# Kernel tuning notes

Hardware: AMD Instinct MI355X
Metric: run time of the kernel (lower is better)

## Reference

```python
import jax, jax.numpy as jnp
import numpy as np

B, S, D = 8, 1024, 1024
H, KV, HD = 16, 16, 64
NDIM = 2
EPS = 1e-6


def rms_norm(x, weight=None, eps=EPS):
    var = jnp.mean(jnp.square(x), axis=-1, keepdims=True)
    out = x * jax.lax.rsqrt(var + eps)
    if weight is not None:
        out = out * weight
    return out


def rotate_half(x):
    half = x.shape[-1] // 2
    return jnp.concatenate((-x[..., half:], x[..., :half]), axis=-1)


def multidim_rope(x, cos, sin, ndim):
    # x: [B,S,H,HD]; cos,sin: [B,S,HD]; head_dim split into ndim contiguous
    # chunks of size per = 2*(HD // (2*ndim)); rotate-half applied per chunk.
    b, s, h, hd = x.shape
    per = 2 * (hd // (2 * ndim))
    xg = x.reshape(b, s, h, ndim, per)
    cg = cos.reshape(b, s, 1, ndim, per)
    sg = sin.reshape(b, s, 1, ndim, per)
    out = xg * cg + rotate_half(xg) * sg
    return out.reshape(b, s, h, hd)


def setup_inputs() -> dict:
    key = jax.random.key(0)
    ks = jax.random.split(key, 10)
    scale = 1.0 / np.sqrt(D)
    return {
        "hidden_states": jax.random.normal(ks[0], (B, S, D), jnp.float32),
        "cos": jax.random.uniform(ks[1], (B, S, HD), jnp.float32, -1.0, 1.0),
        "sin": jax.random.uniform(ks[2], (B, S, HD), jnp.float32, -1.0, 1.0),
        "position_ids": jax.random.randint(ks[3], (B, S, NDIM), 0, 32, jnp.int32),
        "wq": jax.random.normal(ks[4], (D, H * HD), jnp.float32) * scale,
        "wk": jax.random.normal(ks[5], (D, KV * HD), jnp.float32) * scale,
        "wv": jax.random.normal(ks[6], (D, KV * HD), jnp.float32) * scale,
        "wo": jax.random.normal(ks[7], (H * HD, D), jnp.float32) * scale,
        "q_norm_w": jnp.ones((HD,), jnp.float32),
        "k_norm_w": jnp.ones((HD,), jnp.float32),
    }


def reference(hidden_states, cos, sin, position_ids, wq, wk, wv, wo, q_norm_w, k_norm_w):
    b, s, _ = hidden_states.shape
    ndim = position_ids.shape[-1]

    q = (hidden_states @ wq).reshape(b, s, H, HD)
    q = rms_norm(q, q_norm_w)
    q = multidim_rope(q, cos, sin, ndim)

    k = (hidden_states @ wk).reshape(b, s, KV, HD)
    k = rms_norm(k, k_norm_w)
    k = multidim_rope(k, cos, sin, ndim)

    v = (hidden_states @ wv).reshape(b, s, KV, HD)
    v = rms_norm(v, None)  # v_norm has no weight

    # Full (non-causal) vision attention, scaling = 1.0
    scores = jnp.einsum("bqhd,bkhd->bhqk", q, k)
    probs = jax.nn.softmax(scores, axis=-1)
    attn = jnp.einsum("bhqk,bkhd->bqhd", probs, v).reshape(b, s, H * HD)

    return attn @ wo
```

## Files before the change

kernel.cpp:

```cpp
#include <hip/hip_runtime.h>
#include <hip/hip_bf16.h>

typedef __attribute__((ext_vector_type(8))) short bf16x8;
typedef __attribute__((ext_vector_type(4))) short bf16x4;
typedef __attribute__((ext_vector_type(4))) float f32x4;

struct __align__(16) V16 { unsigned long long a, b; };

__device__ __forceinline__ float bf2f(unsigned short u) {
  union { unsigned int i; float f; } c; c.i = ((unsigned int)u) << 16; return c.f;
}
__device__ __forceinline__ unsigned short f2bf(float f) {
  __hip_bfloat16 h = __float2bfloat16(f);
  unsigned short u; __builtin_memcpy(&u, &h, 2); return u;
}

__device__ __forceinline__ void async16(unsigned short* lds,
                                        const unsigned short* g) {
  __builtin_amdgcn_global_load_lds(
      (const __attribute__((address_space(1))) unsigned int*)g,
      (__attribute__((address_space(3))) unsigned int*)lds, 16, 0, 0);
}

#define FP32_MAGIC 0x3F800000u

__global__ __launch_bounds__(256) void cvt_bf16(
    const void* __restrict__ src, size_t srcOff,
    unsigned short* __restrict__ dst, int n4,
    const unsigned int* __restrict__ fmt)
{
  const bool f32 = (fmt[0] == FP32_MAGIC);
  int i = blockIdx.x * blockDim.x + threadIdx.x;
  const int stride = gridDim.x * blockDim.x;
  if (f32) {
    const float* s = (const float*)src + srcOff;
    for (; i < n4; i += stride) {
      float4 v = *(const float4*)(s + (size_t)i * 4);
      ushort2 lo = { f2bf(v.x), f2bf(v.y) };
      ushort2 hi = { f2bf(v.z), f2bf(v.w) };
      *(ushort2*)(dst + (size_t)i * 4)     = lo;
      *(ushort2*)(dst + (size_t)i * 4 + 2) = hi;
    }
  } else {
    const unsigned short* s = (const unsigned short*)src + srcOff;
    for (; i < n4; i += stride) {
      *(ushort4*)(dst + (size_t)i * 4) = *(const ushort4*)(s + (size_t)i * 4);
    }
  }
}

__global__ __launch_bounds__(256) void cvt_t(
    const void* __restrict__ src, unsigned short* __restrict__ dstT,
    const unsigned int* __restrict__ fmt)
{
  __shared__ __align__(16) unsigned short T[64][72];
  const bool f32 = (fmt[0] == FP32_MAGIC);
  const int tid = threadIdx.x;
  const int k0 = blockIdx.x * 64, n0 = blockIdx.y * 64;
  const int rl = tid >> 3, cl = (tid & 7) * 8;

#pragma unroll
  for (int p = 0; p < 2; ++p) {
    int r = rl + p * 32;
    int cs = cl ^ (r & 56);
    if (f32) {
      const float* s = (const float*)src + (size_t)(k0 + r) * 1024 + n0 + cl;
      float4 v0 = *(const float4*)s, v1 = *(const float4*)(s + 4);
      unsigned short* t = &T[r][cs];
      t[0]=f2bf(v0.x); t[1]=f2bf(v0.y); t[2]=f2bf(v0.z); t[3]=f2bf(v0.w);
      t[4]=f2bf(v1.x); t[5]=f2bf(v1.y); t[6]=f2bf(v1.z); t[7]=f2bf(v1.w);
    } else {
      *(V16*)&T[r][cs] = *(const V16*)((const unsigned short*)src +
                                        (size_t)(k0 + r) * 1024 + n0 + cl);
    }
  }
  __syncthreads();

#pragma unroll
  for (int p = 0; p < 2; ++p) {
    int u = tid + p * 256;
    int d = u >> 3, sc = (u & 7) * 8;
    unsigned short tmp[8];
#pragma unroll
    for (int i = 0; i < 8; ++i) tmp[i] = T[sc + i][d ^ sc];
    *(V16*)&dstT[(size_t)(n0 + d) * 1024 + k0 + sc] = *(V16*)tmp;
  }
}

__global__ __launch_bounds__(256) void transpose_v(
    const unsigned short* __restrict__ v, unsigned short* __restrict__ vt)
{
  __shared__ __align__(16) unsigned short T[64][72];
  const int tid = threadIdx.x;
  const int s0 = blockIdx.x * 64;
  const int bh = blockIdx.y;
  const int b = bh >> 4, h = bh & 15;
  const int rl = tid >> 3, cl = (tid & 7) * 8;

#pragma unroll
  for (int p = 0; p < 2; ++p) {
    int r = rl + p * 32;
    *(V16*)&T[r][cl ^ (r & 56)] = *(const V16*)(
        v + (size_t)(b * 1024 + s0 + r) * 1024 + h * 64 + cl);
  }
  __syncthreads();

#pragma unroll
  for (int p = 0; p < 2; ++p) {
    int u = tid + p * 256;
    int d = u >> 3, sc = (u & 7) * 8;
    unsigned short tmp[8];
#pragma unroll
    for (int i = 0; i < 8; ++i) tmp[i] = T[sc + i][d ^ sc];
    *(V16*)&vt[(size_t)(bh * 64 + d) * 1024 + s0 + sc] = *(V16*)tmp;
  }
}

#define TM 128
#define TN 128
#define TK 64

__global__ __launch_bounds__(256) void gemm_qkv(
    const unsigned short* __restrict__ A,
    const unsigned short* __restrict__ Bt,
    unsigned short* __restrict__ Cq,
    unsigned short* __restrict__ Ck,
    unsigned short* __restrict__ Cv,
    const unsigned short* __restrict__ cs,
    const unsigned short* __restrict__ sn,
    const unsigned short* __restrict__ qw,
    const unsigned short* __restrict__ kw,
    int M, int K)
{
  __shared__ __align__(16) unsigned short As[TM][TK];
  __shared__ __align__(16) unsigned short Bs[TN][TK];

  const int tid  = threadIdx.x;
  const int wave = tid >> 6;
  const int lane = tid & 63;
  const int quad = lane >> 4;
  const int l16  = lane & 15;
  const int bm = blockIdx.x * TM;
  const int bn = blockIdx.y * TN;
  const int wm = (wave & 1) * 64;
  const int wn = (wave >> 1) * 64;

  const f32x4 z = {0.f, 0.f, 0.f, 0.f};
  f32x4 acc[4][4];
#pragma unroll
  for (int i = 0; i < 4; ++i)
#pragma unroll
    for (int j = 0; j < 4; ++j) acc[i][j] = z;

  const int lrow = lane >> 3;
  const int gcol = ((lane & 7) ^ lrow) * 8;
  const unsigned short* aP = A  + (size_t)(bm + wave * 8 + lrow) * K + gcol;
  const unsigned short* bP = Bt + (size_t)(bn + wave * 8 + lrow) * K + gcol;
  const int cswz = l16 & 7;

  for (int k0 = 0; k0 < K; k0 += TK) {
#pragma unroll
    for (int p = 0; p < 4; ++p) {
      async16(&As[p * 32 + wave * 8][0], aP + (size_t)p * 32 * K);
      async16(&Bs[p * 32 + wave * 8][0], bP + (size_t)p * 32 * K);
    }
    aP += TK; bP += TK;
    __syncthreads();

#pragma unroll
    for (int s = 0; s < 2; ++s) {
      const int pc = ((s * 4 + quad) ^ cswz) * 8;
      bf16x8 af[4], bfv[4];
#pragma unroll
      for (int mt = 0; mt < 4; ++mt)
        af[mt] = *(const bf16x8*)&As[wm + mt * 16 + l16][pc];
#pragma unroll
      for (int nt = 0; nt < 4; ++nt)
        bfv[nt] = *(const bf16x8*)&Bs[wn + nt * 16 + l16][pc];
#pragma unroll
      for (int mt = 0; mt < 4; ++mt)
#pragma unroll
        for (int nt = 0; nt < 4; ++nt)
          acc[mt][nt] = __builtin_amdgcn_mfma_f32_16x16x32_bf16(
              af[mt], bfv[nt], acc[mt][nt], 0, 0, 0);
    }
    __syncthreads();
  }

  const int which = bn >> 10;
  unsigned short* Cd = (which == 0) ? Cq : (which == 1) ? Ck : Cv;
  const int colbase = (bn & 1023) + wn;

  float wgt[4];
#pragma unroll
  for (int nt = 0; nt < 4; ++nt) {
    int d = nt * 16 + l16;
    wgt[nt] = (which == 0) ? bf2f(qw[d]) * 1.44269504f
            : (which == 1) ? bf2f(kw[d]) : 1.f;
  }

#pragma unroll
  for (int mt = 0; mt < 4; ++mt)
#pragma unroll
    for (int r = 0; r < 4; ++r) {
      const int row = bm + wm + mt * 16 + quad * 4 + r;
      float x0 = acc[mt][0][r], x1 = acc[mt][1][r];
      float x2 = acc[mt][2][r], x3 = acc[mt][3][r];
      float ss = x0 * x0 + x1 * x1 + x2 * x2 + x3 * x3;
      ss += __shfl_xor(ss, 1);
      ss += __shfl_xor(ss, 2);
      ss += __shfl_xor(ss, 4);
      ss += __shfl_xor(ss, 8);
      const float inv = rsqrtf(ss * (1.f / 64.f) + 1e-6f);
      float y[4] = { x0 * inv * wgt[0], x1 * inv * wgt[1],
                     x2 * inv * wgt[2], x3 * inv * wgt[3] };
      float outv[4];
      if (which < 2) {
        const unsigned short* cp = cs + (size_t)row * 64 + l16;
        const unsigned short* sp = sn + (size_t)row * 64 + l16;
#pragma unroll
        for (int nt = 0; nt < 4; ++nt) {
          float c = bf2f(cp[nt * 16]), s = bf2f(sp[nt * 16]);
          float part = (nt & 1) ? y[nt ^ 1] : -y[nt ^ 1];
          outv[nt] = y[nt] * c + part * s;
        }
      } else {
#pragma unroll
        for (int nt = 0; nt < 4; ++nt) outv[nt] = y[nt];
      }
#pragma unroll
      for (int nt = 0; nt < 4; ++nt)
        Cd[(size_t)row * 1024 + colbase + nt * 16 + l16] = f2bf(outv[nt]);
    }
}

__global__ __launch_bounds__(256) void gemm_bf16(
    const unsigned short* __restrict__ A,
    const unsigned short* __restrict__ Bt,
    void* __restrict__ C, size_t cOff,
    const unsigned int* __restrict__ outFmt,
    int M, int N, int K)
{
  __shared__ __align__(16) unsigned short As[TM][TK];
  __shared__ __align__(16) unsigned short Bs[TN][TK];

  const int tid  = threadIdx.x;
  const int wave = tid >> 6;
  const int lane = tid & 63;
  const int quad = lane >> 4;
  const int l16  = lane & 15;
  const int bm = blockIdx.x * TM;
  const int bn = blockIdx.y * TN;
  const int wm = (wave & 1) * 64;
  const int wn = (wave >> 1) * 64;

  const f32x4 z = {0.f, 0.f, 0.f, 0.f};
  f32x4 acc[4][4];
#pragma unroll
  for (int i = 0; i < 4; ++i)
#pragma unroll
    for (int j = 0; j < 4; ++j) acc[i][j] = z;

  const int lrow = lane >> 3;
  const int gcol = ((lane & 7) ^ lrow) * 8;
  const unsigned short* aP = A  + (size_t)(bm + wave * 8 + lrow) * K + gcol;
  const unsigned short* bP = Bt + (size_t)(bn + wave * 8 + lrow) * K + gcol;
  const int cswz = l16 & 7;

  for (int k0 = 0; k0 < K; k0 += TK) {
#pragma unroll
    for (int p = 0; p < 4; ++p) {
      async16(&As[p * 32 + wave * 8][0], aP + (size_t)p * 32 * K);
      async16(&Bs[p * 32 + wave * 8][0], bP + (size_t)p * 32 * K);
    }
    aP += TK; bP += TK;
    __syncthreads();

#pragma unroll
    for (int s = 0; s < 2; ++s) {
      const int pc = ((s * 4 + quad) ^ cswz) * 8;
      bf16x8 af[4], bfv[4];
#pragma unroll
      for (int mt = 0; mt < 4; ++mt)
        af[mt] = *(const bf16x8*)&As[wm + mt * 16 + l16][pc];
#pragma unroll
      for (int nt = 0; nt < 4; ++nt)
        bfv[nt] = *(const bf16x8*)&Bs[wn + nt * 16 + l16][pc];
#pragma unroll
      for (int mt = 0; mt < 4; ++mt)
#pragma unroll
        for (int nt = 0; nt < 4; ++nt)
          acc[mt][nt] = __builtin_amdgcn_mfma_f32_16x16x32_bf16(
              af[mt], bfv[nt], acc[mt][nt], 0, 0, 0);
    }
    __syncthreads();
  }

  const bool of32 = (outFmt != nullptr) && (outFmt[0] == FP32_MAGIC);
  float* Cf = (float*)C + cOff;
  unsigned short* Ch = (unsigned short*)C + cOff;

#pragma unroll
  for (int mt = 0; mt < 4; ++mt)
#pragma unroll
    for (int nt = 0; nt < 4; ++nt)
#pragma unroll
      for (int r = 0; r < 4; ++r) {
        int row = bm + wm + mt * 16 + quad * 4 + r;
        int col = bn + wn + nt * 16 + l16;
        size_t idx = (size_t)row * N + col;
        if (of32) Cf[idx] = acc[mt][nt][r];
        else      Ch[idx] = f2bf(acc[mt][nt][r]);
      }
}

__global__ __launch_bounds__(256) void attn_fused(
    const unsigned short* __restrict__ q,
    const unsigned short* __restrict__ k,
    const unsigned short* __restrict__ vt,
    unsigned short* __restrict__ o)
{
  __shared__ __align__(16) unsigned short Ks[2][64][64];
  __shared__ __align__(16) unsigned short Vs[2][64][64];

  const int tid  = threadIdx.x;
  const int wave = tid >> 6;
  const int lane = tid & 63;
  const int quad = lane >> 4;
  const int l16  = lane & 15;
  const int bh = blockIdx.y;
  const int b  = bh >> 4, h = bh & 15;
  const int qbase = blockIdx.x * 64 + wave * 16;
  const size_t bbase = (size_t)b * 1024;

  bf16x8 qf[2];
  {
    const unsigned short* qp = q + (bbase + qbase + l16) * 1024 + h * 64;
    qf[0] = *(const bf16x8*)(qp + quad * 8);
    qf[1] = *(const bf16x8*)(qp + 32 + quad * 8);
  }

  const f32x4 z = {0.f, 0.f, 0.f, 0.f};
  f32x4 of[5];
#pragma unroll
  for (int nt = 0; nt < 5; ++nt) of[nt] = z;
  float m_run = -1e30f;

  const bf16x8 onesv = { 0x3F80, 0x3F80, 0x3F80, 0x3F80,
                         0x3F80, 0x3F80, 0x3F80, 0x3F80 };

  const int lrow = lane >> 3;
  const int gcol = ((lane & 7) ^ lrow) * 8;
  const unsigned short* kP = k  + (bbase + wave * 8 + lrow) * 1024 + h * 64 + gcol;
  const unsigned short* vP = vt + ((size_t)bh * 64 + wave * 8 + lrow) * 1024 + gcol;
  const int cswz = l16 & 7;

  auto STAGE = [&](int buf, int kt) {
#pragma unroll
    for (int p = 0; p < 2; ++p) {
      async16(&Ks[buf][p * 32 + wave * 8][0], kP + ((size_t)kt * 64 + p * 32) * 1024);
      async16(&Vs[buf][p * 32 + wave * 8][0], vP + (size_t)p * 32 * 1024 + kt * 64);
    }
  };

  STAGE(0, 0);
  __syncthreads();

  for (int kt = 0; kt < 16; ++kt) {
    const int cur = kt & 1;
    if (kt < 15) STAGE(cur ^ 1, kt + 1);

    f32x4 sf[4];
#pragma unroll
    for (int nt = 0; nt < 4; ++nt) sf[nt] = z;
#pragma unroll
    for (int s = 0; s < 2; ++s) {
      const int pc = ((s * 4 + quad) ^ cswz) * 8;
#pragma unroll
      for (int nt = 0; nt < 4; ++nt) {
        bf16x8 kf = *(const bf16x8*)&Ks[cur][nt * 16 + l16][pc];
        sf[nt] = __builtin_amdgcn_mfma_f32_16x16x32_bf16(kf, qf[s], sf[nt], 0, 0, 0);
      }
    }

    float m0 = fmaxf(fmaxf(sf[0][0], sf[0][1]), fmaxf(sf[0][2], sf[0][3]));
    float m1 = fmaxf(fmaxf(sf[1][0], sf[1][1]), fmaxf(sf[1][2], sf[1][3]));
    float m2 = fmaxf(fmaxf(sf[2][0], sf[2][1]), fmaxf(sf[2][2], sf[2][3]));
    float m3 = fmaxf(fmaxf(sf[3][0], sf[3][1]), fmaxf(sf[3][2], sf[3][3]));
    float mx = fmaxf(fmaxf(m0, m1), fmaxf(m2, m3));
    mx = fmaxf(mx, __shfl_xor(mx, 16));
    mx = fmaxf(mx, __shfl_xor(mx, 32));

    if (!__all(mx - m_run <= 11.5f)) {
      float mn = fmaxf(m_run, mx);
      float alpha = __builtin_amdgcn_exp2f(m_run - mn);
      m_run = mn;
      float ar[4];
#pragma unroll
      for (int r = 0; r < 4; ++r) ar[r] = __shfl(alpha, quad * 4 + r);
#pragma unroll
      for (int nt = 0; nt < 5; ++nt)
#pragma unroll
        for (int r = 0; r < 4; ++r) of[nt][r] *= ar[r];
    }

    bf16x8 pf[2];
#pragma unroll
    for (int nt = 0; nt < 4; ++nt)
#pragma unroll
      for (int r = 0; r < 4; ++r)
        pf[nt >> 1][(nt & 1) * 4 + r] =
            (short)f2bf(__builtin_amdgcn_exp2f(sf[nt][r] - m_run));

#pragma unroll
    for (int s = 0; s < 2; ++s) {
#pragma unroll
      for (int nt = 0; nt < 4; ++nt) {
        const unsigned short* vrow = &Vs[cur][nt * 16 + l16][0];
        const int g0  = (4 * s + (quad >> 1)) ^ cswz;
        const int off = 4 * (quad & 1);
        bf16x4 v0 = *(const bf16x4*)(vrow + g0 * 8 + off);
        bf16x4 v1 = *(const bf16x4*)(vrow + (g0 ^ 2) * 8 + off);
        bf16x8 vf = __builtin_shufflevector(v0, v1, 0, 1, 2, 3, 4, 5, 6, 7);
        of[nt] = __builtin_amdgcn_mfma_f32_16x16x32_bf16(pf[s], vf, of[nt], 0, 0, 0);
      }
      of[4] = __builtin_amdgcn_mfma_f32_16x16x32_bf16(pf[s], onesv, of[4], 0, 0, 0);
    }

    __syncthreads();
  }

  float invl[4];
#pragma unroll
  for (int r = 0; r < 4; ++r) invl[r] = 1.f / of[4][r];
#pragma unroll
  for (int nt = 0; nt < 4; ++nt)
#pragma unroll
    for (int r = 0; r < 4; ++r) {
      int row = qbase + quad * 4 + r;
      o[(bbase + row) * 1024 + h * 64 + nt * 16 + l16] = f2bf(of[nt][r] * invl[r]);
    }
}

extern "C" void kernel_launch(void* const* d_in, const int* in_sizes, int n_in,
                              void* d_out, int out_size, void* d_ws, size_t ws_size,
                              hipStream_t stream) {
  const void* hidden = d_in[0];
  const void* cosr   = d_in[1];
  const void* sinr   = d_in[2];
  const void* wq     = d_in[4];
  const void* wk     = d_in[5];
  const void* wv     = d_in[6];
  const void* wo     = d_in[7];
  const void* qnw    = d_in[8];
  const void* knw    = d_in[9];
  const unsigned int* fmt = (const unsigned int*)qnw;

  const size_t MEG = 1024 * 1024;
  dim3 blk(256);
  unsigned short* w = (unsigned short*)d_ws;

  auto cvt = [&](const void* src, size_t srcOff, unsigned short* dst, int n) {
    int n4 = n / 4;
    int blocks = (n4 + 1023) / 1024;
    if (blocks > 2048) blocks = 2048;
    cvt_bf16<<<dim3(blocks), blk, 0, stream>>>(src, srcOff, dst, n4, fmt);
  };
  auto cvtT = [&](const void* src, unsigned short* dstT) {
    cvt_t<<<dim3(16, 16), blk, 0, stream>>>(src, dstT, fmt);
  };

  if (ws_size >= (size_t)60 * MEG) {
    unsigned short* hb   = w;
    unsigned short* vtb  = w;
    unsigned short* wqT  = w + 8 * MEG;
    unsigned short* wkT  = w + 9 * MEG;
    unsigned short* wvT  = w + 10 * MEG;
    unsigned short* woT  = w + 11 * MEG;
    unsigned short* csb  = w + 12 * MEG;
    unsigned short* snb  = w + 12 * MEG + 512 * 1024;
    unsigned short* qnb  = w + 13 * MEG;
    unsigned short* knb  = w + 13 * MEG + 64;
    unsigned short* qb   = w + 14 * MEG;
    unsigned short* kb   = w + 22 * MEG;
    unsigned short* vb   = (unsigned short*)d_out;
    unsigned short* ab   = qb;

    cvt(hidden, 0, hb, 8 * MEG);
    cvtT(wq, wqT);  cvtT(wk, wkT);  cvtT(wv, wvT);  cvtT(wo, woT);
    cvt(cosr, 0, csb, 512 * 1024);  cvt(sinr, 0, snb, 512 * 1024);
    cvt(qnw, 0, qnb, 64);  cvt(knw, 0, knb, 64);

    const int M = 8192, K = 1024;
    gemm_qkv<<<dim3(M / TM, 24), blk, 0, stream>>>(hb, wqT, qb, kb, vb,
                                                   csb, snb, qnb, knb, M, K);
    transpose_v<<<dim3(16, 8 * 16), blk, 0, stream>>>(vb, vtb);
    attn_fused<<<dim3(16, 8 * 16), blk, 0, stream>>>(qb, kb, vtb, ab);
    gemm_bf16<<<dim3(M / TM, 8), blk, 0, stream>>>(ab, woT, d_out, 0, fmt,
                                                   M, 1024, K);
  } else {
    unsigned short* wqT  = w;
    unsigned short* wkT  = w + 1 * MEG;
    unsigned short* wvT  = w + 2 * MEG;
    unsigned short* woT  = w + 3 * MEG;
    unsigned short* csb  = w + 4 * MEG;
    unsigned short* snb  = w + 4 * MEG + 512 * 1024;
    unsigned short* qnb  = w + 5 * MEG;
    unsigned short* knb  = w + 5 * MEG + 64;
    unsigned short* hbb  = w + 6 * MEG;
    unsigned short* qb   = w + 7 * MEG;
    unsigned short* kb   = w + 8 * MEG;
    unsigned short* vb   = w + 9 * MEG;
    unsigned short* vtb  = w + 10 * MEG;

    cvtT(wq, wqT);  cvtT(wk, wkT);  cvtT(wv, wvT);  cvtT(wo, woT);
    cvt(cosr, 0, csb, 512 * 1024);  cvt(sinr, 0, snb, 512 * 1024);
    cvt(qnw, 0, qnb, 64);  cvt(knw, 0, knb, 64);

    const int Mb = 1024, K = 1024;
    for (int b = 0; b < 8; ++b) {
      cvt(hidden, (size_t)b * MEG, hbb, MEG);
      gemm_qkv<<<dim3(Mb / TM, 24), blk, 0, stream>>>(
          hbb, wqT, qb, kb, vb, csb + (size_t)b * 64 * 1024,
          snb + (size_t)b * 64 * 1024, qnb, knb, Mb, K);
      transpose_v<<<dim3(16, 16), blk, 0, stream>>>(vb, vtb);
      attn_fused<<<dim3(16, 16), blk, 0, stream>>>(qb, kb, vtb, qb);
      gemm_bf16<<<dim3(Mb / TM, 8), blk, 0, stream>>>(qb, woT, d_out,
                                                      (size_t)b * MEG, fmt,
                                                      Mb, 1024, K);
    }
  }
}
```

Before: 306.0 us.

## Double-buffer GEMM loads, batch conversion launches, add MFMA priority hints

```diff
diff --git a/kernel.cpp b/kernel.cpp
--- a/kernel.cpp
+++ b/kernel.cpp
@@ -11,8 +11,9 @@
   union { unsigned int i; float f; } c; c.i = ((unsigned int)u) << 16; return c.f;
 }
 __device__ __forceinline__ unsigned short f2bf(float f) {
-  __hip_bfloat16 h = __float2bfloat16(f);
-  unsigned short u; __builtin_memcpy(&u, &h, 2); return u;
+  unsigned int u; __builtin_memcpy(&u, &f, 4);
+  u += 0x7FFFu + ((u >> 16) & 1u);
+  return (unsigned short)(u >> 16);
 }
 
 __device__ __forceinline__ void async16(unsigned short* lds,
@@ -24,16 +25,12 @@
 
 #define FP32_MAGIC 0x3F800000u
 
-__global__ __launch_bounds__(256) void cvt_bf16(
-    const void* __restrict__ src, size_t srcOff,
-    unsigned short* __restrict__ dst, int n4,
-    const unsigned int* __restrict__ fmt)
-{
-  const bool f32 = (fmt[0] == FP32_MAGIC);
-  int i = blockIdx.x * blockDim.x + threadIdx.x;
-  const int stride = gridDim.x * blockDim.x;
+__device__ __forceinline__ void cvt_seg(
+    const void* __restrict__ src, unsigned short* __restrict__ dst,
+    int n4, int i, int stride, bool f32)
+{
   if (f32) {
-    const float* s = (const float*)src + srcOff;
+    const float* s = (const float*)src;
     for (; i < n4; i += stride) {
       float4 v = *(const float4*)(s + (size_t)i * 4);
       ushort2 lo = { f2bf(v.x), f2bf(v.y) };
@@ -42,18 +39,61 @@
       *(ushort2*)(dst + (size_t)i * 4 + 2) = hi;
     }
   } else {
-    const unsigned short* s = (const unsigned short*)src + srcOff;
-    for (; i < n4; i += stride) {
+    const unsigned short* s = (const unsigned short*)src;
+    for (; i < n4; i += stride)
       *(ushort4*)(dst + (size_t)i * 4) = *(const ushort4*)(s + (size_t)i * 4);
-    }
-  }
-}
-
-__global__ __launch_bounds__(256) void cvt_t(
-    const void* __restrict__ src, unsigned short* __restrict__ dstT,
+  }
+}
+
+__global__ __launch_bounds__(256) void cvt_bf16(
+    const void* __restrict__ src, size_t srcOff,
+    unsigned short* __restrict__ dst, int n4,
     const unsigned int* __restrict__ fmt)
 {
+  const bool f32 = (fmt[0] == FP32_MAGIC);
+  const int i = blockIdx.x * blockDim.x + threadIdx.x;
+  const int stride = gridDim.x * blockDim.x;
+  const void* s = f32 ? (const void*)((const float*)src + srcOff)
+                      : (const void*)((const unsigned short*)src + srcOff);
+  cvt_seg(s, dst, n4, i, stride, f32);
+}
+
+__global__ __launch_bounds__(256) void cvt_all(
+    const void* __restrict__ hid, const void* __restrict__ cosr,
+    const void* __restrict__ sinr, const void* __restrict__ qnw,
+    const void* __restrict__ knw,
+    unsigned short* __restrict__ hb, unsigned short* __restrict__ csb,
+    unsigned short* __restrict__ snb, unsigned short* __restrict__ qnb,
+    unsigned short* __restrict__ knb,
+    int hidden_n4, const unsigned int* __restrict__ fmt)
+{
+  const bool f32 = (fmt[0] == FP32_MAGIC);
+  const int bx = blockIdx.x, tid = threadIdx.x;
+  if (bx < 2048) {
+    if (hidden_n4 > 0)
+      cvt_seg(hid, hb, hidden_n4, bx * 256 + tid, 2048 * 256, f32);
+  } else if (bx < 2176) {
+    cvt_seg(cosr, csb, 131072, (bx - 2048) * 256 + tid, 128 * 256, f32);
+  } else if (bx < 2304) {
+    cvt_seg(sinr, snb, 131072, (bx - 2176) * 256 + tid, 128 * 256, f32);
+  } else {
+    if (tid < 16)       cvt_seg(qnw, qnb, 16, tid, 16, f32);
+    else if (tid < 32)  cvt_seg(knw, knb, 16, tid - 16, 16, f32);
+  }
+}
+
+__global__ __launch_bounds__(256) void cvt_t4(
+    const void* __restrict__ s0, const void* __restrict__ s1,
+    const void* __restrict__ s2, const void* __restrict__ s3,
+    unsigned short* __restrict__ d0, unsigned short* __restrict__ d1,
+    unsigned short* __restrict__ d2, unsigned short* __restrict__ d3,
+    const unsigned int* __restrict__ fmt)
+{
   __shared__ __align__(16) unsigned short T[64][72];
+  const int z = blockIdx.z;
+  const void* src = (z == 0) ? s0 : (z == 1) ? s1 : (z == 2) ? s2 : s3;
+  unsigned short* dstT = (z == 0) ? d0 : (z == 1) ? d1 : (z == 2) ? d2 : d3;
+
   const bool f32 = (fmt[0] == FP32_MAGIC);
   const int tid = threadIdx.x;
   const int k0 = blockIdx.x * 64, n0 = blockIdx.y * 64;
@@ -119,6 +159,7 @@
 #define TM 128
 #define TN 128
 #define TK 64
+#define GK 1024
 
 __global__ __launch_bounds__(256) void gemm_qkv(
     const unsigned short* __restrict__ A,
@@ -130,10 +171,10 @@
     const unsigned short* __restrict__ sn,
     const unsigned short* __restrict__ qw,
     const unsigned short* __restrict__ kw,
-    int M, int K)
-{
-  __shared__ __align__(16) unsigned short As[TM][TK];
-  __shared__ __align__(16) unsigned short Bs[TN][TK];
+    int M)
+{
+  __shared__ __align__(16) unsigned short As[2][TM][TK];
+  __shared__ __align__(16) unsigned short Bs[2][TN][TK];
 
   const int tid  = threadIdx.x;
   const int wave = tid >> 6;
@@ -154,29 +195,35 @@
 
   const int lrow = lane >> 3;
   const int gcol = ((lane & 7) ^ lrow) * 8;
-  const unsigned short* aP = A  + (size_t)(bm + wave * 8 + lrow) * K + gcol;
-  const unsigned short* bP = Bt + (size_t)(bn + wave * 8 + lrow) * K + gcol;
+  const unsigned short* aP = A  + (size_t)(bm + wave * 8 + lrow) * GK + gcol;
+  const unsigned short* bP = Bt + (size_t)(bn + wave * 8 + lrow) * GK + gcol;
   const int cswz = l16 & 7;
 
-  for (int k0 = 0; k0 < K; k0 += TK) {
+  auto STAGE = [&](int buf, int t) {
 #pragma unroll
     for (int p = 0; p < 4; ++p) {
-      async16(&As[p * 32 + wave * 8][0], aP + (size_t)p * 32 * K);
-      async16(&Bs[p * 32 + wave * 8][0], bP + (size_t)p * 32 * K);
-    }
-    aP += TK; bP += TK;
-    __syncthreads();
-
+      async16(&As[buf][p * 32 + wave * 8][0], aP + t * TK + p * 32 * GK);
+      async16(&Bs[buf][p * 32 + wave * 8][0], bP + t * TK + p * 32 * GK);
+    }
+  };
+
+  STAGE(0, 0);
+  __syncthreads();
+
+#pragma unroll 2
+  for (int t = 0; t < GK / TK; ++t) {
+    const int cur = t & 1;
+    if (t < GK / TK - 1) STAGE(cur ^ 1, t + 1);
 #pragma unroll
     for (int s = 0; s < 2; ++s) {
       const int pc = ((s * 4 + quad) ^ cswz) * 8;
       bf16x8 af[4], bfv[4];
 #pragma unroll
       for (int mt = 0; mt < 4; ++mt)
-        af[mt] = *(const bf16x8*)&As[wm + mt * 16 + l16][pc];
+        af[mt] = *(const bf16x8*)&As[cur][wm + mt * 16 + l16][pc];
 #pragma unroll
       for (int nt = 0; nt < 4; ++nt)
-        bfv[nt] = *(const bf16x8*)&Bs[wn + nt * 16 + l16][pc];
+        bfv[nt] = *(const bf16x8*)&Bs[cur][wn + nt * 16 + l16][pc];
 #pragma unroll
       for (int mt = 0; mt < 4; ++mt)
 #pragma unroll
@@ -239,10 +286,10 @@
     const unsigned short* __restrict__ Bt,
     void* __restrict__ C, size_t cOff,
     const unsigned int* __restrict__ outFmt,
-    int M, int N, int K)
-{
-  __shared__ __align__(16) unsigned short As[TM][TK];
-  __shared__ __align__(16) unsigned short Bs[TN][TK];
+    int M, int N)
+{
+  __shared__ __align__(16) unsigned short As[2][TM][TK];
+  __shared__ __align__(16) unsigned short Bs[2][TN][TK];
 
   const int tid  = threadIdx.x;
   const int wave = tid >> 6;
@@ -263,29 +310,35 @@
 
   const int lrow = lane >> 3;
   const int gcol = ((lane & 7) ^ lrow) * 8;
-  const unsigned short* aP = A  + (size_t)(bm + wave * 8 + lrow) * K + gcol;
-  const unsigned short* bP = Bt + (size_t)(bn + wave * 8 + lrow) * K + gcol;
+  const unsigned short* aP = A  + (size_t)(bm + wave * 8 + lrow) * GK + gcol;
+  const unsigned short* bP = Bt + (size_t)(bn + wave * 8 + lrow) * GK + gcol;
   const int cswz = l16 & 7;
 
-  for (int k0 = 0; k0 < K; k0 += TK) {
+  auto STAGE = [&](int buf, int t) {
 #pragma unroll
     for (int p = 0; p < 4; ++p) {
-      async16(&As[p * 32 + wave * 8][0], aP + (size_t)p * 32 * K);
-      async16(&Bs[p * 32 + wave * 8][0], bP + (size_t)p * 32 * K);
-    }
-    aP += TK; bP += TK;
-    __syncthreads();
-
+      async16(&As[buf][p * 32 + wave * 8][0], aP + t * TK + p * 32 * GK);
+      async16(&Bs[buf][p * 32 + wave * 8][0], bP + t * TK + p * 32 * GK);
+    }
+  };
+
+  STAGE(0, 0);
+  __syncthreads();
+
+#pragma unroll 2
+  for (int t = 0; t < GK / TK; ++t) {
+    const int cur = t & 1;
+    if (t < GK / TK - 1) STAGE(cur ^ 1, t + 1);
 #pragma unroll
     for (int s = 0; s < 2; ++s) {
       const int pc = ((s * 4 + quad) ^ cswz) * 8;
       bf16x8 af[4], bfv[4];
 #pragma unroll
       for (int mt = 0; mt < 4; ++mt)
-        af[mt] = *(const bf16x8*)&As[wm + mt * 16 + l16][pc];
+        af[mt] = *(const bf16x8*)&As[cur][wm + mt * 16 + l16][pc];
 #pragma unroll
       for (int nt = 0; nt < 4; ++nt)
-        bfv[nt] = *(const bf16x8*)&Bs[wn + nt * 16 + l16][pc];
+        bfv[nt] = *(const bf16x8*)&Bs[cur][wn + nt * 16 + l16][pc];
 #pragma unroll
       for (int mt = 0; mt < 4; ++mt)
 #pragma unroll
@@ -366,6 +419,7 @@
   STAGE(0, 0);
   __syncthreads();
 
+#pragma unroll 2
   for (int kt = 0; kt < 16; ++kt) {
     const int cur = kt & 1;
     if (kt < 15) STAGE(cur ^ 1, kt + 1);
@@ -373,6 +427,7 @@
     f32x4 sf[4];
 #pragma unroll
     for (int nt = 0; nt < 4; ++nt) sf[nt] = z;
+    __builtin_amdgcn_s_setprio(1);
 #pragma unroll
     for (int s = 0; s < 2; ++s) {
       const int pc = ((s * 4 + quad) ^ cswz) * 8;
@@ -382,6 +437,7 @@
         sf[nt] = __builtin_amdgcn_mfma_f32_16x16x32_bf16(kf, qf[s], sf[nt], 0, 0, 0);
       }
     }
+    __builtin_amdgcn_s_setprio(0);
 
     float m0 = fmaxf(fmaxf(sf[0][0], sf[0][1]), fmaxf(sf[0][2], sf[0][3]));
     float m1 = fmaxf(fmaxf(sf[1][0], sf[1][1]), fmaxf(sf[1][2], sf[1][3]));
@@ -412,6 +468,7 @@
         pf[nt >> 1][(nt & 1) * 4 + r] =
             (short)f2bf(__builtin_amdgcn_exp2f(sf[nt][r] - m_run));
 
+    __builtin_amdgcn_s_setprio(1);
 #pragma unroll
     for (int s = 0; s < 2; ++s) {
 #pragma unroll
@@ -426,6 +483,7 @@
       }
       of[4] = __builtin_amdgcn_mfma_f32_16x16x32_bf16(pf[s], onesv, of[4], 0, 0, 0);
     }
+    __builtin_amdgcn_s_setprio(0);
 
     __syncthreads();
   }
@@ -459,16 +517,6 @@
   const size_t MEG = 1024 * 1024;
   dim3 blk(256);
   unsigned short* w = (unsigned short*)d_ws;
-
-  auto cvt = [&](const void* src, size_t srcOff, unsigned short* dst, int n) {
-    int n4 = n / 4;
-    int blocks = (n4 + 1023) / 1024;
-    if (blocks > 2048) blocks = 2048;
-    cvt_bf16<<<dim3(blocks), blk, 0, stream>>>(src, srcOff, dst, n4, fmt);
-  };
-  auto cvtT = [&](const void* src, unsigned short* dstT) {
-    cvt_t<<<dim3(16, 16), blk, 0, stream>>>(src, dstT, fmt);
-  };
 
   if (ws_size >= (size_t)60 * MEG) {
     unsigned short* hb   = w;
@@ -486,18 +534,19 @@
     unsigned short* vb   = (unsigned short*)d_out;
     unsigned short* ab   = qb;
 
-    cvt(hidden, 0, hb, 8 * MEG);
-    cvtT(wq, wqT);  cvtT(wk, wkT);  cvtT(wv, wvT);  cvtT(wo, woT);
-    cvt(cosr, 0, csb, 512 * 1024);  cvt(sinr, 0, snb, 512 * 1024);
-    cvt(qnw, 0, qnb, 64);  cvt(knw, 0, knb, 64);
-
-    const int M = 8192, K = 1024;
+    cvt_all<<<dim3(2305), blk, 0, stream>>>(hidden, cosr, sinr, qnw, knw,
+                                            hb, csb, snb, qnb, knb,
+                                            2 * (int)MEG, fmt);
+    cvt_t4<<<dim3(16, 16, 4), blk, 0, stream>>>(wq, wk, wv, wo,
+                                                wqT, wkT, wvT, woT, fmt);
+
+    const int M = 8192;
     gemm_qkv<<<dim3(M / TM, 24), blk, 0, stream>>>(hb, wqT, qb, kb, vb,
-                                                   csb, snb, qnb, knb, M, K);
+                                                   csb, snb, qnb, knb, M);
     transpose_v<<<dim3(16, 8 * 16), blk, 0, stream>>>(vb, vtb);
     attn_fused<<<dim3(16, 8 * 16), blk, 0, stream>>>(qb, kb, vtb, ab);
     gemm_bf16<<<dim3(M / TM, 8), blk, 0, stream>>>(ab, woT, d_out, 0, fmt,
-                                                   M, 1024, K);
+                                                   M, 1024);
   } else {
     unsigned short* wqT  = w;
     unsigned short* wkT  = w + 1 * MEG;
@@ -513,21 +562,24 @@
     unsigned short* vb   = w + 9 * MEG;
     unsigned short* vtb  = w + 10 * MEG;
 
-    cvtT(wq, wqT);  cvtT(wk, wkT);  cvtT(wv, wvT);  cvtT(wo, woT);
-    cvt(cosr, 0, csb, 512 * 1024);  cvt(sinr, 0, snb, 512 * 1024);
-    cvt(qnw, 0, qnb, 64);  cvt(knw, 0, knb, 64);
-
-    const int Mb = 1024, K = 1024;
+    cvt_t4<<<dim3(16, 16, 4), blk, 0, stream>>>(wq, wk, wv, wo,
+                                                wqT, wkT, wvT, woT, fmt);
+    cvt_all<<<dim3(2305), blk, 0, stream>>>(hidden, cosr, sinr, qnw, knw,
+                                            nullptr, csb, snb, qnb, knb,
+                                            0, fmt);
+
+    const int Mb = 1024;
     for (int b = 0; b < 8; ++b) {
-      cvt(hidden, (size_t)b * MEG, hbb, MEG);
+      cvt_bf16<<<dim3(512), blk, 0, stream>>>(hidden, (size_t)b * MEG, hbb,
+                                              (int)(MEG / 4), fmt);
       gemm_qkv<<<dim3(Mb / TM, 24), blk, 0, stream>>>(
           hbb, wqT, qb, kb, vb, csb + (size_t)b * 64 * 1024,
-          snb + (size_t)b * 64 * 1024, qnb, knb, Mb, K);
+          snb + (size_t)b * 64 * 1024, qnb, knb, Mb);
       transpose_v<<<dim3(16, 16), blk, 0, stream>>>(vb, vtb);
       attn_fused<<<dim3(16, 16), blk, 0, stream>>>(qb, kb, vtb, qb);
       gemm_bf16<<<dim3(Mb / TM, 8), blk, 0, stream>>>(qb, woT, d_out,
                                                       (size_t)b * MEG, fmt,
-                                                      Mb, 1024, K);
-    }
-  }
-}
+                                                      Mb, 1024);
+    }
+  }
+}
```

After: 286.5 us. 6.4% less time.
